# Kernel optimization log

Measured on AMD Instinct MI355X. Metric: run time of the kernel, lower is better.

## Reference

```python
import jax, jax.numpy as jnp
import numpy as np

R, T, N, OPS = 3, 3, 50000, 24
E, B, MAXDEG = 400000, 32, 8
QD, ED, H = 128, 128, 128


def lstm_scan(x, Wih, Whh, bih, bhh):
    # x: (T, B, D). PyTorch LSTM gate order: i, f, g, o.
    Hh = Whh.shape[-1]
    def step(carry, xt):
        h, c = carry
        g = xt @ Wih.T + bih + h @ Whh.T + bhh
        i, f, gg, o = jnp.split(g, 4, axis=-1)
        c = jax.nn.sigmoid(f) * c + jax.nn.sigmoid(i) * jnp.tanh(gg)
        h = jax.nn.sigmoid(o) * jnp.tanh(c)
        return (h, c), h
    z = jnp.zeros((x.shape[1], Hh), x.dtype)
    (hT, _), ys = jax.lax.scan(step, (z, z), x)
    return ys, hT


def bilstm(x, Wih, Whh, bih, bhh):
    # weights have a leading direction axis of size 2 (fwd, bwd)
    ys_f, h_f = lstm_scan(x, Wih[0], Whh[0], bih[0], bhh[0])
    ys_b, h_b = lstm_scan(x[::-1], Wih[1], Whh[1], bih[1], bhh[1])
    return jnp.concatenate([ys_f, ys_b[::-1]], -1), jnp.concatenate([h_f, h_b], -1)


def setup_inputs() -> dict:
    key = jax.random.key(0)
    ks = jax.random.split(key, 20)
    s = 0.05
    inp = {}
    inp["queries"] = jax.random.randint(ks[0], (B,), 0, OPS)
    inp["heads"] = jax.random.randint(ks[1], (B,), 0, N)
    inp["rels"] = jax.random.randint(ks[2], (E,), 0, OPS // 2)
    inp["t_heads"] = jax.random.randint(ks[3], (E,), 0, N)
    inp["t_tails"] = jax.random.randint(ks[4], (E,), 0, N)
    inp["entity_degrees"] = jax.random.randint(ks[5], (N, MAXDEG), 0, OPS + 1)
    inp["query_embedding"] = jax.random.normal(ks[6], (OPS, QD)) * s
    ent = jax.random.normal(ks[7], (OPS + 1, ED)) * s
    inp["entity_embedding"] = ent.at[OPS].set(0.0)  # padding_idx row is zero
    inp["q_Wih"] = jax.random.normal(ks[8], (R, 2, 4 * H, QD)) * s
    inp["q_Whh"] = jax.random.normal(ks[9], (R, 2, 4 * H, H)) * s
    inp["q_bih"] = jax.random.normal(ks[10], (R, 2, 4 * H)) * s
    inp["q_bhh"] = jax.random.normal(ks[11], (R, 2, 4 * H)) * s
    inp["e_Wih"] = jax.random.normal(ks[12], (2, 4 * H, ED)) * s
    inp["e_Whh"] = jax.random.normal(ks[13], (2, 4 * H, H)) * s
    inp["e_bih"] = jax.random.normal(ks[14], (2, 4 * H)) * s
    inp["e_bhh"] = jax.random.normal(ks[15], (2, 4 * H)) * s
    inp["q_lin_W"] = jax.random.normal(ks[16], (OPS + 1, 2 * H)) * s
    inp["q_lin_b"] = jax.random.normal(ks[17], (OPS + 1,)) * s
    inp["e_lin_W"] = jax.random.normal(ks[18], (OPS, 2 * H)) * s
    inp["e_lin_b"] = jax.random.normal(ks[19], (OPS,)) * s
    return inp


def reference(queries, heads, rels, t_heads, t_tails, entity_degrees,
              query_embedding, entity_embedding, q_Wih, q_Whh, q_bih, q_bhh,
              e_Wih, e_Whh, e_bih, e_bhh, q_lin_W, q_lin_b, e_lin_W, e_lin_b):
    # --- query attention over operators, one BiLSTM per rank ---
    qx = jnp.broadcast_to(query_embedding[queries][None], (T, B, QD))  # (T, B, QD)
    def q_branch(Wih, Whh, bih, bhh):
        ys, _ = bilstm(qx, Wih, Whh, bih, bhh)                 # (T, B, 2H)
        return jax.nn.softmax(ys @ q_lin_W.T + q_lin_b, axis=-1)  # (T, B, OPS+1)
    query_attn = jax.vmap(q_branch)(q_Wih, q_Whh, q_bih, q_bhh)   # (R, T, B, OPS+1)

    # --- entity attention from degree-sequence BiLSTM (final hidden states) ---
    ex = entity_embedding[entity_degrees].transpose(1, 0, 2)      # (MAXDEG, N, ED)
    _, e_h = bilstm(ex, e_Wih, e_Whh, e_bih, e_bhh)               # (N, 2H)
    entity_attn = jax.nn.softmax(e_h @ e_lin_W.T + e_lin_b, axis=-1)  # (N, OPS)

    # sparse operator values: A_rel[h, t] = entity_attn[h, rel] for fact (rel, h, t)
    w = entity_attn[t_heads, rels]  # (E,)
    half = OPS // 2

    logits = jnp.zeros((B, N), jnp.float32)
    for r in range(R):
        memory = jax.nn.one_hot(heads, N, dtype=jnp.float32)  # (B, N)
        for t in range(T):
            qa = query_attn[r, t]  # (B, OPS+1)
            # forward op: (memory @ A_rel), weighted by qa[rel]
            fwd = (qa[:, rels] * w[None, :]) * memory[:, t_heads]        # (B, E)
            # reverse op: (memory @ A_rel.T), weighted by qa[rel + half]
            rev = (qa[:, rels + half] * w[None, :]) * memory[:, t_tails]  # (B, E)
            added = (jnp.zeros((B, N), jnp.float32)
                     .at[:, t_tails].add(fwd)
                     .at[:, t_heads].add(rev))
            added = added + memory * qa[:, -1:]
            memory = added / jnp.maximum(1e-20, added.sum(axis=1, keepdims=True))
        logits = logits + memory
    return logits
```

## Files before the change

### kernel.cpp

```cpp
#include <hip/hip_runtime.h>

#define R_ 3
#define T_ 3
#define N_ 50000
#define OPS_ 24
#define E_ 400000
#define B_ 32
#define MAXDEG_ 8
#define QD_ 128
#define ED_ 128
#define H_ 128
#define G4_ (4*H_)
#define HPAD 168
#define PSLOTS 64
#define RB_ 96

#define WB_ ((2*32*5*64*8 + 511) / 512)
#define CB_ ((E_ + 511) / 512)
#define BF_ ((E_ + 511) / 512)
#define ZU_ 586
#define ZM_ 25
#define ZS_ 12
#define EB_ 16

#define QB_ (R_ * B_)
#define SCANBLK_ ((N_ + 31) / 32)
#define BF2E_ ((E_ + 511) / 512)
#define BF2N_ ((N_ + 511) / 512)

typedef unsigned short u16;
typedef unsigned char u8;
typedef __attribute__((ext_vector_type(8))) short bf16x8;
typedef __attribute__((ext_vector_type(8))) _Float16 f16x8;
typedef __attribute__((ext_vector_type(4))) float f32x4;

#define BF16_ONE ((short)0x3F80)
#define LOG2E_  1.44269504f
#define LOG2E2_ 2.88539008f

__device__ __forceinline__ short f2bf(float f){
  union { float f; unsigned u; } v; v.f = f;
  unsigned r = v.u + 0x7fffu + ((v.u >> 16) & 1u);
  return (short)(r >> 16);
}
__device__ __forceinline__ float bf2f(u16 u){
  union { unsigned u; float f; } v; v.u = ((unsigned)u) << 16; return v.f;
}
__device__ __forceinline__ float frcp(float x){ return __builtin_amdgcn_rcpf(x); }
__device__ __forceinline__ float fsig(float x){ return frcp(1.0f + __expf(-x)); }
__device__ __forceinline__ float ftanh(float x){
  return __builtin_fmaf(2.0f, fsig(2.0f * x), -1.0f);
}
__device__ __forceinline__ float fexp2(float x){
#if __has_builtin(__builtin_amdgcn_exp2f)
  return __builtin_amdgcn_exp2f(x);
#else
  return __expf(x * 0.6931471806f);
#endif
}

__device__ void qattn_body(int bid, const int* __restrict__ queries, const float* __restrict__ qemb,
    const float* __restrict__ qWih, const float* __restrict__ qWhh,
    const float* __restrict__ qbih, const float* __restrict__ qbhh,
    const float* __restrict__ qlinW, const float* __restrict__ qlinb,
    float* __restrict__ query_attn )
{
  int r = bid / B_;
  int b = bid % B_;
  int tid = threadIdx.x;
  int d   = tid >> 8;
  int t2  = tid & 255;
  __shared__ float x[QD_];
  __shared__ float gx[2][G4_];
  __shared__ float h[2][H_], c[2][H_];
  __shared__ float gtmp[2][G4_];
  __shared__ float hh[2][T_][H_];
  __shared__ float lg[OPS_ + 1];

  int q = queries[b];
  if (tid < QD_) x[tid] = qemb[q * QD_ + tid];
  __syncthreads();

  const float* Wih = qWih + (size_t)(r * 2 + d) * G4_ * QD_;
  const float* Whh = qWhh + (size_t)(r * 2 + d) * G4_ * H_;
  const float* bih = qbih + (r * 2 + d) * G4_;
  const float* bhh = qbhh + (r * 2 + d) * G4_;
  for (int j = t2; j < G4_; j += 256){
    const float4* wr = (const float4*)(Wih + (size_t)j * QD_);
    float s = bih[j] + bhh[j];
    for (int k = 0; k < QD_ / 4; ++k){
      float4 wv = wr[k];
      s += wv.x * x[4*k] + wv.y * x[4*k+1] + wv.z * x[4*k+2] + wv.w * x[4*k+3];
    }
    gx[d][j] = s;
  }
  if (t2 < H_){ h[d][t2] = 0.f; c[d][t2] = 0.f; }
  __syncthreads();
  for (int t = 0; t < T_; ++t){
    for (int j = t2; j < G4_; j += 256){
      const float4* wr = (const float4*)(Whh + (size_t)j * H_);
      float s = 0.f;
      for (int k = 0; k < H_ / 4; ++k){
        float4 wv = wr[k];
        s += wv.x * h[d][4*k] + wv.y * h[d][4*k+1] + wv.z * h[d][4*k+2] + wv.w * h[d][4*k+3];
      }
      gtmp[d][j] = gx[d][j] + s;
    }
    __syncthreads();
    if (t2 < H_){
      float gi = gtmp[d][t2], gf = gtmp[d][t2 + H_], gg = gtmp[d][t2 + 2*H_], go = gtmp[d][t2 + 3*H_];
      float cn = fsig(gf) * c[d][t2] + fsig(gi) * ftanh(gg);
      float hn = fsig(go) * ftanh(cn);
      c[d][t2] = cn; h[d][t2] = hn;
      hh[d][t][t2] = hn;
    }
    __syncthreads();
  }

  for (int t = 0; t < T_; ++t){
    if (tid < OPS_ + 1){
      const float* wr = qlinW + tid * (2 * H_);
      float s = qlinb[tid];
      for (int k = 0; k < H_; ++k) s += wr[k] * hh[0][t][k];
      for (int k = 0; k < H_; ++k) s += wr[H_ + k] * hh[1][T_ - 1 - t][k];
      lg[tid] = s;
    }
    __syncthreads();
    if (tid == 0){
      float m = -1e30f;
      for (int o = 0; o < OPS_ + 1; ++o) m = fmaxf(m, lg[o]);
      float sum = 0.f;
      for (int o = 0; o < OPS_ + 1; ++o){ float e = __expf(lg[o] - m); lg[o] = e; sum += e; }
      float inv = frcp(sum);
      for (int o = 0; o < OPS_ + 1; ++o) lg[o] *= inv;
    }
    __syncthreads();
    if (tid < OPS_ + 1) query_attn[((size_t)(r * T_ + t) * B_ + b) * (OPS_ + 1) + tid] = lg[tid];
    __syncthreads();
  }
}

__device__ void wbuild_body(int bid, const float* __restrict__ eWhh,
                            const float* __restrict__ eemb, const float* __restrict__ eWih,
                            const float* __restrict__ ebih, const float* __restrict__ ebhh,
                            u16* __restrict__ wtile, u16* __restrict__ wonehot)
{
  int idx = bid * 512 + threadIdx.x;
  if (idx >= 2 * 32 * 5 * 64 * 8) return;
  int jj = idx & 7;
  int lane = (idx >> 3) & 63;
  int kc = (idx >> 9) % 5;
  int gtile = (idx / (8 * 64 * 5)) & 31;
  int dir = idx / (8 * 64 * 5 * 32);
  int row = lane >> 4, col = lane & 15;
  int j = gtile * 16 + col;
  float sc = ((gtile >> 3) == 2) ? LOG2E2_ : LOG2E_;
  if (kc < 4){
    int k = kc * 32 + row * 8 + jj;
    float v = eWhh[((size_t)dir * G4_ + j) * H_ + k] * sc;
    wtile[((((size_t)dir * 32 + gtile) * 4 + kc) * 64 + lane) * 8 + jj] = (u16)f2bf(v);
  } else {
    int vdeg = row * 8 + jj;
    float v = 0.f;
    if (vdeg <= OPS_){
      const float4* wr = (const float4*)(eWih + (size_t)(dir * G4_ + j) * ED_);
      const float4* er = (const float4*)(eemb + (size_t)vdeg * ED_);
      float s = ebih[dir * G4_ + j] + ebhh[dir * G4_ + j];
      for (int k = 0; k < ED_ / 4; ++k){
        float4 wv = wr[k], ev = er[k];
        s += wv.x * ev.x + wv.y * ev.y + wv.z * ev.z + wv.w * ev.w;
      }
      v = s * sc;
    }
    wonehot[(((size_t)dir * 32 + gtile) * 64 + lane) * 8 + jj] = (u16)f2bf(v);
  }
}

__device__ void csr_count_body(int bid, const int* __restrict__ theads,
                               const int* __restrict__ ttails, int* __restrict__ counts)
{
  int e = bid * 512 + threadIdx.x;
  if (e < E_){
    atomicAdd(&counts[ttails[e]], 1);
    atomicAdd(&counts[theads[e]], 1);
  }
}

__device__ void bfs1_body(int bid, const int* __restrict__ heads,
                          const int* __restrict__ theads, const int* __restrict__ ttails,
                          u8* __restrict__ hs1)
{
  if (bid == 0 && threadIdx.x < B_) hs1[heads[threadIdx.x]] = 1;
  int e = bid * 512 + threadIdx.x;
  if (e < E_){
    int a = theads[e], t = ttails[e];
    #pragma unroll 8
    for (int i = 0; i < B_; ++i){
      int hd = heads[i];
      if (a == hd) hs1[t] = 1;
      if (t == hd) hs1[a] = 1;
    }
  }
}

__global__ __launch_bounds__(512) void front_kernel(
    const float* eWhh, const float* eemb, const float* eWih,
    const float* ebih, const float* ebhh, u16* wtile, u16* wonehot,
    const int* theads, const int* ttails, int* counts,
    const int* heads, u8* hs1,
    float* u2, int* maski, float* sumsP,
    const float* elinW, u16* etile)
{
  int bid = blockIdx.x;
  int tid = threadIdx.x;
  if (bid < WB_){
    wbuild_body(bid, eWhh, eemb, eWih, ebih, ebhh, wtile, wonehot);
  } else if (bid < WB_ + CB_){
    csr_count_body(bid - WB_, theads, ttails, counts);
  } else if (bid < WB_ + CB_ + BF_){
    bfs1_body(bid - WB_ - CB_, heads, theads, ttails, hs1);
  } else if (bid < WB_ + CB_ + BF_ + ZU_){
    int zb = bid - WB_ - CB_ - BF_;
    float4 z = {0.f, 0.f, 0.f, 0.f};
    size_t base = (size_t)zb * 8192 + tid * 4;
    #pragma unroll
    for (int k = 0; k < 4; ++k){
      size_t idx = base + (size_t)k * 2048;
      if (idx < (size_t)N_ * RB_) *(float4*)&u2[idx] = z;
    }
  } else if (bid < WB_ + CB_ + BF_ + ZU_ + ZM_){
    int mi = (bid - WB_ - CB_ - BF_ - ZU_) * 512 + tid;
    if (mi < (N_ + 3) / 4) maski[mi] = 0;
  } else if (bid < WB_ + CB_ + BF_ + ZU_ + ZM_ + ZS_){
    int si = (bid - WB_ - CB_ - BF_ - ZU_ - ZM_) * 512 + tid;
    if (si < PSLOTS * RB_) sumsP[si] = 0.f;
  } else {
    int idx = (bid - (WB_ + CB_ + BF_ + ZU_ + ZM_ + ZS_)) * 512 + tid;
    if (idx < 8192){
      int jj = idx & 7;
      int lane = (idx >> 3) & 63;
      int ks = (idx >> 9) & 7;
      int ot = idx >> 12;
      int op = ot * 16 + (lane & 15);
      int k  = ks * 32 + (lane >> 4) * 8 + jj;
      float v = (op < OPS_) ? elinW[(size_t)op * (2 * H_) + k] : 0.f;
      _Float16 hv = (_Float16)v;
      etile[idx] = *(const u16*)&hv;
    }
  }
}

__device__ void bfs2_body(int bid, const int* __restrict__ theads,
                          const int* __restrict__ ttails,
                          const u8* __restrict__ hs1, u8* __restrict__ mask)
{
  if (bid < BF2E_){
    int e = bid * 512 + threadIdx.x;
    if (e < E_){
      int a = theads[e], t = ttails[e];
      if (hs1[a]) mask[t] = 1;
      if (hs1[t]) mask[a] = 1;
    }
  } else {
    int n = (bid - BF2E_) * 512 + threadIdx.x;
    if (n < N_ && hs1[n]) mask[n] = 1;
  }
}

__device__ void scan_body(const int* __restrict__ counts, int* __restrict__ rowptr,
                          int* __restrict__ cursor, int* __restrict__ cursor2)
{
  __shared__ int wsum[8];
  int t = threadIdx.x;
  int lane = t & 63, wv = t >> 6;
  int carry = 0;
  for (int base = 0; base < N_; base += 2048){
    int idx = base + t * 4;
    int c0 = 0, c1 = 0, c2 = 0, c3 = 0;
    if (idx + 3 < N_){
      int4 c = *(const int4*)&counts[idx];
      c0 = c.x; c1 = c.y; c2 = c.z; c3 = c.w;
    } else {
      if (idx     < N_) c0 = counts[idx];
      if (idx + 1 < N_) c1 = counts[idx + 1];
      if (idx + 2 < N_) c2 = counts[idx + 2];
      if (idx + 3 < N_) c3 = counts[idx + 3];
    }
    int s = c0 + c1 + c2 + c3;
    int sc = s;
    #pragma unroll
    for (int off = 1; off < 64; off <<= 1){
      int v = __shfl_up(sc, off);
      if (lane >= off) sc += v;
    }
    if (lane == 63) wsum[wv] = sc;
    __syncthreads();
    if (t == 0){
      int acc = carry;
      #pragma unroll
      for (int w = 0; w < 8; ++w){ int v = wsum[w]; wsum[w] = acc; acc += v; }
      carry = acc;
    }
    __syncthreads();
    int excl = wsum[wv] + (sc - s);
    int r0 = excl, r1 = r0 + c0, r2 = r1 + c1, r3 = r2 + c2;
    if (idx + 3 < N_){
      int4 rv; rv.x = r0; rv.y = r1; rv.z = r2; rv.w = r3;
      *(int4*)&rowptr[idx]  = rv;
      *(int4*)&cursor[idx]  = rv;
      *(int4*)&cursor2[idx] = rv;
    } else {
      if (idx     < N_){ rowptr[idx]   = r0; cursor[idx]   = r0; cursor2[idx]   = r0; }
      if (idx + 1 < N_){ rowptr[idx+1] = r1; cursor[idx+1] = r1; cursor2[idx+1] = r1; }
      if (idx + 2 < N_){ rowptr[idx+2] = r2; cursor[idx+2] = r2; cursor2[idx+2] = r2; }
      if (idx + 3 < N_){ rowptr[idx+3] = r3; cursor[idx+3] = r3; cursor2[idx+3] = r3; }
    }
  }
  if (t == 0) rowptr[N_] = carry;
}

__global__ __launch_bounds__(512, 4) void elstm_kernel(
    const int* __restrict__ degs,
    const u16* __restrict__ wtile, const u16* __restrict__ wonehot,
    const u16* __restrict__ etile, const float* __restrict__ elinb,
    float* __restrict__ attn ,
    const int* __restrict__ counts, int* __restrict__ rowptr,
    int* __restrict__ cursor, int* __restrict__ cursor2,
    const int* __restrict__ theads, const int* __restrict__ ttails,
    const u8* __restrict__ hs1, u8* __restrict__ mask,
    const int* __restrict__ queries, const float* __restrict__ qemb,
    const float* __restrict__ qWih, const float* __restrict__ qWhh,
    const float* __restrict__ qbih, const float* __restrict__ qbhh,
    const float* __restrict__ qlinW, const float* __restrict__ qlinb,
    float* __restrict__ query_attn)
{
  int bid = blockIdx.x;
  if (bid < QB_){
    qattn_body(bid, queries, qemb, qWih, qWhh, qbih, qbhh, qlinW, qlinb, query_attn);
    return;
  }
  int eb = bid - QB_;
  if (eb >= SCANBLK_){
    int rid = eb - SCANBLK_;
    if (rid == 0) scan_body(counts, rowptr, cursor, cursor2);
    else          bfs2_body(rid - 1, theads, ttails, hs1, mask);
    return;
  }

  int tid = threadIdx.x;
  int lane = tid & 63;
  int w = tid >> 6;
  int wu = __builtin_amdgcn_readfirstlane(w);
  int row = lane >> 4, col = lane & 15;
  int ebase = eb * 32;

  __shared__ __align__(16) short hl[2][32 * HPAD];
  __shared__ __align__(16) short hfin[32 * 136];
  __shared__ float lgs[32][33];

  int eg0 = ebase + tid; if (eg0 >= N_) eg0 = N_ - 1;

  for (int i = tid; i < 2 * 32 * HPAD; i += 512) ((short*)hl)[i] = 0;
  __syncthreads();
  if (tid < 32) hl[0][tid * HPAD + H_ + degs[(size_t)eg0 * MAXDEG_ + 0]] = BF16_ONE;
  __syncthreads();

  int swzr = (col >> 2) & 3;

  for (int dir = 0; dir < 2; ++dir){
    const u16* Wt  = wtile   + (size_t)dir * 32 * 4 * 64 * 8;
    const u16* Woh = wonehot + (size_t)dir * 32 * 64 * 8;
    const u16* W0 = Wt + (size_t)((0 * 8 + wu) * 4 * 64) * 8;
    const u16* W1 = Wt + (size_t)((1 * 8 + wu) * 4 * 64) * 8;
    const u16* W2 = Wt + (size_t)((2 * 8 + wu) * 4 * 64) * 8;
    const u16* W3 = Wt + (size_t)((3 * 8 + wu) * 4 * 64) * 8;
    const u16* O0 = Woh + (size_t)((0 * 8 + wu) * 64) * 8;
    const u16* O1 = Woh + (size_t)((1 * 8 + wu) * 64) * 8;
    const u16* O2 = Woh + (size_t)((2 * 8 + wu) * 64) * 8;
    const u16* O3 = Woh + (size_t)((3 * 8 + wu) * 64) * 8;
    float cst[8];
    #pragma unroll
    for (int i = 0; i < 8; ++i) cst[i] = 0.f;

    for (int t = 0; t < MAXDEG_; ++t){
      const short* hb = hl[t & 1];
      short*       hw = hl[(t + 1) & 1];
      f32x4 acc[8];
      #pragma unroll
      for (int i = 0; i < 8; ++i) acc[i] = (f32x4){0.f, 0.f, 0.f, 0.f};

      #pragma unroll 2
      for (int kc = 0; kc < 4; ++kc){
        bf16x8 af0 = *(const bf16x8*)&hb[(col) * HPAD + kc * 32 + (row ^ swzr) * 8];
        bf16x8 af1 = *(const bf16x8*)&hb[(16 + col) * HPAD + kc * 32 + (row ^ swzr) * 8];
        int lo = (kc * 64 + lane) * 8;
        bf16x8 b0 = *(const bf16x8*)(W0 + lo);
        bf16x8 b1 = *(const bf16x8*)(W1 + lo);
        bf16x8 b2 = *(const bf16x8*)(W2 + lo);
        bf16x8 b3 = *(const bf16x8*)(W3 + lo);
        acc[0] = __builtin_amdgcn_mfma_f32_16x16x32_bf16(af0, b0, acc[0], 0, 0, 0);
        acc[1] = __builtin_amdgcn_mfma_f32_16x16x32_bf16(af1, b0, acc[1], 0, 0, 0);
        acc[2] = __builtin_amdgcn_mfma_f32_16x16x32_bf16(af0, b1, acc[2], 0, 0, 0);
        acc[3] = __builtin_amdgcn_mfma_f32_16x16x32_bf16(af1, b1, acc[3], 0, 0, 0);
        acc[4] = __builtin_amdgcn_mfma_f32_16x16x32_bf16(af0, b2, acc[4], 0, 0, 0);
        acc[5] = __builtin_amdgcn_mfma_f32_16x16x32_bf16(af1, b2, acc[5], 0, 0, 0);
        acc[6] = __builtin_amdgcn_mfma_f32_16x16x32_bf16(af0, b3, acc[6], 0, 0, 0);
        acc[7] = __builtin_amdgcn_mfma_f32_16x16x32_bf16(af1, b3, acc[7], 0, 0, 0);
      }
      {
        bf16x8 af0 = *(const bf16x8*)&hb[(col) * HPAD + H_ + row * 8];
        bf16x8 af1 = *(const bf16x8*)&hb[(16 + col) * HPAD + H_ + row * 8];
        int lo = lane * 8;
        bf16x8 b0 = *(const bf16x8*)(O0 + lo);
        bf16x8 b1 = *(const bf16x8*)(O1 + lo);
        bf16x8 b2 = *(const bf16x8*)(O2 + lo);
        bf16x8 b3 = *(const bf16x8*)(O3 + lo);
        acc[0] = __builtin_amdgcn_mfma_f32_16x16x32_bf16(af0, b0, acc[0], 0, 0, 0);
        acc[1] = __builtin_amdgcn_mfma_f32_16x16x32_bf16(af1, b0, acc[1], 0, 0, 0);
        acc[2] = __builtin_amdgcn_mfma_f32_16x16x32_bf16(af0, b1, acc[2], 0, 0, 0);
        acc[3] = __builtin_amdgcn_mfma_f32_16x16x32_bf16(af1, b1, acc[3], 0, 0, 0);
        acc[4] = __builtin_amdgcn_mfma_f32_16x16x32_bf16(af0, b2, acc[4], 0, 0, 0);
        acc[5] = __builtin_amdgcn_mfma_f32_16x16x32_bf16(af1, b2, acc[5], 0, 0, 0);
        acc[6] = __builtin_amdgcn_mfma_f32_16x16x32_bf16(af0, b3, acc[6], 0, 0, 0);
        acc[7] = __builtin_amdgcn_mfma_f32_16x16x32_bf16(af1, b3, acc[7], 0, 0, 0);
      }

      #pragma unroll
      for (int mt = 0; mt < 2; ++mt){
        #pragma unroll
        for (int reg = 0; reg < 4; ++reg){
          int e = mt * 16 + row * 4 + reg;
          int jsw = (((wu * 2 + (col >> 3)) ^ row) * 8) + (col & 7);
          float Gi = acc[0 + mt][reg];
          float Gf = acc[2 + mt][reg];
          float Gg = acc[4 + mt][reg];
          float Go = acc[6 + mt][reg];
          int ci = mt * 4 + reg;
          float ea = fexp2(-Gi);
          float ef = fexp2(-Gf);
          float eb2 = fexp2(-Gg);
          float eo = fexp2(-Go);
          float t1 = 1.f + ef, t2 = 1.f + ea, t3 = 1.f + eb2;
          float p = t2 * t3;
          float num = __builtin_fmaf(cst[ci], p, (1.f - eb2) * t1);
          float cn = num * frcp(t1 * p);
          float ed = fexp2(cn * (-LOG2E2_));
          float hn = (1.f - ed) * frcp((1.f + eo) * (1.f + ed));
          cst[ci] = cn;
          hw[e * HPAD + jsw] = f2bf(hn);
        }
      }
      if (tid < 32){
        const int* dr = degs + (size_t)eg0 * MAXDEG_;
        if (t >= 1)
          hw[tid * HPAD + H_ + dr[dir ? (MAXDEG_ - t) : (t - 1)]] = 0;
        if (t < MAXDEG_ - 1)
          hw[tid * HPAD + H_ + dr[dir ? (MAXDEG_ - 2 - t) : (t + 1)]] = BF16_ONE;
      }
      __syncthreads();
    }

    if (dir == 0){
      for (int i = tid; i < 32 * 16; i += 512){
        int e = i >> 4, c = i & 15;
        int sz = (e >> 2) & 3;
        *(bf16x8*)&hfin[e * 136 + c * 8] =
            *(const bf16x8*)&hl[0][e * HPAD + ((c ^ sz) * 8)];
      }
      __syncthreads();
      for (int i = tid; i < 2 * 32 * HPAD; i += 512) ((short*)hl)[i] = 0;
      __syncthreads();
      if (tid < 32) hl[0][tid * HPAD + H_ + degs[(size_t)eg0 * MAXDEG_ + (MAXDEG_ - 1)]] = BF16_ONE;
      __syncthreads();
    }
  }

  if (wu < 4){
    int mt = wu >> 1, ot = wu & 1;
    int e2 = mt * 16 + col;
    f32x4 accL = (f32x4){0.f, 0.f, 0.f, 0.f};
    #pragma unroll
    for (int ks = 0; ks < 8; ++ks){
      bf16x8 ra;
      if (ks < 4) ra = *(const bf16x8*)&hfin[e2 * 136 + ks * 32 + row * 8];
      else        ra = *(const bf16x8*)&hl[0][e2 * HPAD + (ks - 4) * 32 + (row ^ swzr) * 8];
      f16x8 af;
      #pragma unroll
      for (int jj = 0; jj < 8; ++jj) af[jj] = (_Float16)bf2f((u16)ra[jj]);
      f16x8 bfr = *(const f16x8*)(etile + (((size_t)(ot * 8 + ks)) * 64 + lane) * 8);
      accL = __builtin_amdgcn_mfma_f32_16x16x32_f16(af, bfr, accL, 0, 0, 0);
    }
    #pragma unroll
    for (int reg = 0; reg < 4; ++reg){
      int ent = mt * 16 + (lane >> 4) * 4 + reg;
      int op  = ot * 16 + (lane & 15);
      float bb = (op < OPS_) ? elinb[op] : 0.f;
      lgs[ent][op] = accL[reg] + bb;
    }
  }
  __syncthreads();
  if (tid < 32){
    int n = ebase + tid;
    if (n < N_){
      float m = -1e30f;
      #pragma unroll
      for (int o = 0; o < OPS_; ++o) m = fmaxf(m, lgs[tid][o]);
      float s = 0.f;
      #pragma unroll
      for (int o = 0; o < OPS_; ++o) s += __expf(lgs[tid][o] - m);
      float inv = frcp(s);
      #pragma unroll
      for (int o = 0; o < OPS_; ++o)
        attn[(size_t)n * OPS_ + o] = __expf(lgs[tid][o] - m) * inv;
    }
  }
}

__global__ void csr_fill_kernel(const int* __restrict__ rels, const int* __restrict__ theads,
                                const int* __restrict__ ttails, const float* __restrict__ attn,
                                const u8* __restrict__ mask, const u8* __restrict__ hs1,
                                int* __restrict__ cursor, int* __restrict__ cursor2,
                                uint2* __restrict__ ents, uint2* __restrict__ ents2)
{
  int e = blockIdx.x * 256 + threadIdx.x;
  if (e < E_){
    int hh = theads[e], tt = ttails[e];
    int mh = mask[hh], mt = mask[tt];
    if (!(mh | mt)) return;
    int rel = rels[e];
    unsigned wb = __float_as_uint(attn[(size_t)hh * OPS_ + rel]);
    if (mh){
      uint2 v1; v1.x = (unsigned)hh | ((unsigned)rel << 16); v1.y = wb;
      ents[atomicAdd(&cursor[tt], 1)] = v1;
    }
    if (mt){
      uint2 v2; v2.x = (unsigned)tt | ((unsigned)(rel + OPS_/2) << 16); v2.y = wb;
      ents[atomicAdd(&cursor[hh], 1)] = v2;
    }
    if (hs1[hh]){
      uint2 w1; w1.x = (unsigned)tt | ((unsigned)rel << 16); w1.y = wb;
      ents2[atomicAdd(&cursor2[hh], 1)] = w1;
    }
    if (hs1[tt]){
      uint2 w2; w2.x = (unsigned)hh | ((unsigned)(rel + OPS_/2) << 16); w2.y = wb;
      ents2[atomicAdd(&cursor2[tt], 1)] = w2;
    }
  }
}

__global__ void t01_kernel(const int* __restrict__ heads, const float* __restrict__ query_attn,
                           const int* __restrict__ rowptr, const int* __restrict__ cend2,
                           const uint2* __restrict__ ents2, float* __restrict__ u2)
{
  __shared__ float qa0[OPS_ + 1], qa1[OPS_ + 1];
  int blk = blockIdx.x;
  int r = blk >> 5, b = blk & 31;
  int rb = r * 32 + b;
  int tid = threadIdx.x;
  if (tid < OPS_ + 1){
    qa0[tid] = query_attn[((size_t)(r * T_ + 0) * B_ + b) * (OPS_ + 1) + tid];
    qa1[tid] = query_attn[((size_t)(r * T_ + 1) * B_ + b) * (OPS_ + 1) + tid];
  }
  __syncthreads();
  int hd = heads[b];
  int beg = rowptr[hd], end = cend2[hd];
  float q024 = qa0[OPS_], q124 = qa1[OPS_];
  if (tid == 0) atomicAdd(&u2[(size_t)hd * RB_ + rb], q124 * q024);
  for (int i = beg + tid; i < end; i += 64){
    uint2 e1 = ents2[i];
    int s  = (int)(e1.x & 0xFFFFu);
    int r1 = (int)(e1.x >> 16);
    float w1 = __uint_as_float(e1.y);
    atomicAdd(&u2[(size_t)s * RB_ + rb], w1 * (q124 * qa0[r1] + qa1[r1] * q024));
    float v1 = qa0[r1] * w1;
    int b2 = rowptr[s], e2e = cend2[s];
    for (int jj = b2; jj < e2e; ++jj){
      uint2 e2 = ents2[jj];
      int d2 = (int)(e2.x & 0xFFFFu);
      int r2 = (int)(e2.x >> 16);
      atomicAdd(&u2[(size_t)d2 * RB_ + rb], qa1[r2] * __uint_as_float(e2.y) * v1);
    }
  }
}

__global__ __launch_bounds__(256) void gather3_kernel(
    const float* __restrict__ ucur, float* __restrict__ unxt,
    const float* __restrict__ query_attn, int t,
    const int* __restrict__ rowptr, const int* __restrict__ cend,
    const uint2* __restrict__ ents, const u8* __restrict__ mask,
    float* __restrict__ partial )
{
  __shared__ float qas[3 * B_ * (OPS_ + 1)];
  __shared__ float red[RB_];
  int tid = threadIdx.x;
  for (int i = tid; i < 3 * B_ * (OPS_ + 1); i += 256){
    int r = i / (B_ * (OPS_ + 1));
    int rem = i - r * (B_ * (OPS_ + 1));
    qas[i] = query_attn[(size_t)(r * T_ + t) * B_ * (OPS_ + 1) + rem];
  }
  if (tid < RB_) red[tid] = 0.f;
  __syncthreads();
  int b   = tid & 31;
  int hw2 = tid >> 5;
  const float* q0 = &qas[0 * 800 + b * (OPS_ + 1)];
  const float* q1 = &qas[1 * 800 + b * (OPS_ + 1)];
  const float* q2 = &qas[2 * 800 + b * (OPS_ + 1)];
  float s0a = 0.f, s1a = 0.f, s2a = 0.f;
  for (int n = blockIdx.x * 8 + hw2; n < N_; n += gridDim.x * 8){
    int beg = rowptr[n], end = cend[n];
    int mk = mask[n];
    if (end == beg && !mk) continue;
    size_t nb = (size_t)n * RB_;
    float a0 = 0.f, a1 = 0.f, a2 = 0.f;
    if (mk){
      a0 = ucur[nb + b]      * q0[OPS_];
      a1 = ucur[nb + 32 + b] * q1[OPS_];
      a2 = ucur[nb + 64 + b] * q2[OPS_];
    }
    #pragma unroll 2
    for (int i = beg; i < end; ++i){
      uint2 e0 = ents[i];
      size_t s0 = (size_t)(e0.x & 0xFFFFu) * RB_;
      int r0 = (int)(e0.x >> 16);
      float w0 = __uint_as_float(e0.y);
      a0 += q0[r0] * w0 * ucur[s0 + b];
      a1 += q1[r0] * w0 * ucur[s0 + 32 + b];
      a2 += q2[r0] * w0 * ucur[s0 + 64 + b];
    }
    unxt[nb + b]      = a0;
    unxt[nb + 32 + b] = a1;
    unxt[nb + 64 + b] = a2;
    s0a += a0; s1a += a1; s2a += a2;
  }
  atomicAdd(&red[b], s0a);
  atomicAdd(&red[32 + b], s1a);
  atomicAdd(&red[64 + b], s2a);
  __syncthreads();
  if (tid < RB_)
    atomicAdd(&partial[(blockIdx.x & (PSLOTS - 1)) * RB_ + tid], red[tid]);
}

__global__ void fintrans_kernel(const float* __restrict__ u, const float* __restrict__ partial,
                                const int* __restrict__ rowptr, const int* __restrict__ cend,
                                const u8* __restrict__ mask,
                                float* __restrict__ out)
{
  __shared__ float sinv[RB_];
  __shared__ float t[B_][72];
  int tid = threadIdx.x;
  if (tid < RB_){
    float s = 0.f;
    #pragma unroll 8
    for (int k = 0; k < PSLOTS; ++k) s += partial[k * RB_ + tid];
    sinv[tid] = frcp(fmaxf(1e-20f, s));
  }
  __syncthreads();
  int n0 = blockIdx.x * 64;
  for (int i = tid; i < 64 * B_; i += 256){
    int nl = i >> 5, b = i & 31;
    int n = n0 + nl;
    float v = 0.f;
    if (n < N_ && (mask[n] || cend[n] > rowptr[n])){
      size_t nb = (size_t)n * RB_;
      v = u[nb + b] * sinv[b] + u[nb + 32 + b] * sinv[32 + b] + u[nb + 64 + b] * sinv[64 + b];
    }
    t[b][nl] = v;
  }
  __syncthreads();
  for (int i = tid; i < 64 * B_; i += 256){
    int b = i >> 6, nl = i & 63;
    int n = n0 + nl;
    if (n < N_) out[(size_t)b * N_ + n] = t[b][nl];
  }
}

extern "C" void kernel_launch(void* const* d_in, const int* in_sizes, int n_in,
                              void* d_out, int out_size, void* d_ws, size_t ws_size,
                              hipStream_t stream)
{
  const int*   queries = (const int*)d_in[0];
  const int*   heads   = (const int*)d_in[1];
  const int*   rels    = (const int*)d_in[2];
  const int*   t_heads = (const int*)d_in[3];
  const int*   t_tails = (const int*)d_in[4];
  const int*   edeg    = (const int*)d_in[5];
  const float* qemb    = (const float*)d_in[6];
  const float* eemb    = (const float*)d_in[7];
  const float* qWih    = (const float*)d_in[8];
  const float* qWhh    = (const float*)d_in[9];
  const float* qbih    = (const float*)d_in[10];
  const float* qbhh    = (const float*)d_in[11];
  const float* eWih    = (const float*)d_in[12];
  const float* eWhh    = (const float*)d_in[13];
  const float* ebih    = (const float*)d_in[14];
  const float* ebhh    = (const float*)d_in[15];
  const float* qlinW   = (const float*)d_in[16];
  const float* qlinb   = (const float*)d_in[17];
  const float* elinW   = (const float*)d_in[18];
  const float* elinb   = (const float*)d_in[19];
  float* out = (float*)d_out;

  char* ws = (char*)d_ws;
  size_t off = 0;
  auto alloc = [&](size_t bytes){ void* p = ws + off; off += (bytes + 255) & ~(size_t)255; return p; };
  char*  bigB  = (char*)alloc((size_t)N_ * RB_ * 4);
  float* attn  = (float*)bigB;
  float* u3    = (float*)bigB;
  uint2* ents       = (uint2*)alloc((size_t)2 * E_ * 8);
  float* u2         = (float*)alloc((size_t)N_ * RB_ * 4);
  uint2* ents2      = (uint2*)alloc((size_t)2 * E_ * 8);
  float* query_attn = (float*)alloc((size_t)R_ * T_ * B_ * (OPS_ + 1) * 4);
  u16*   wtile      = (u16*)  alloc((size_t)2 * 32 * 4 * 64 * 8 * 2);
  u16*   wonehot    = (u16*)  alloc((size_t)2 * 32 * 64 * 8 * 2);
  u16*   etile      = (u16*)  alloc((size_t)2 * 8 * 64 * 8 * 2);
  int*   counts     = (int*)  alloc((size_t)(N_ + 1) * 4);
  int*   rowptr     = (int*)  alloc((size_t)(N_ + 1) * 4);
  int*   cursor     = (int*)  alloc((size_t)(N_ + 1) * 4);
  int*   cursor2    = (int*)  alloc((size_t)(N_ + 1) * 4);
  u8*    hs1        = (u8*)   alloc((size_t)N_);
  u8*    mask       = (u8*)   alloc((size_t)N_);
  float* sumsP      = (float*)alloc((size_t)PSLOTS * RB_ * 4);

  hipMemsetAsync(counts, 0, (size_t)(N_ + 1) * 4, stream);
  hipMemsetAsync(hs1, 0, (size_t)N_, stream);

  front_kernel<<<WB_ + CB_ + BF_ + ZU_ + ZM_ + ZS_ + EB_, 512, 0, stream>>>(
      eWhh, eemb, eWih, ebih, ebhh, wtile, wonehot,
      t_heads, t_tails, counts, heads, hs1, u2, (int*)mask, sumsP, elinW, etile);
  elstm_kernel<<<QB_ + SCANBLK_ + 1 + BF2E_ + BF2N_, 512, 0, stream>>>(
      edeg, wtile, wonehot, etile, elinb, attn,
      counts, rowptr, cursor, cursor2,
      t_heads, t_tails, hs1, mask,
      queries, qemb, qWih, qWhh, qbih, qbhh, qlinW, qlinb, query_attn);
  csr_fill_kernel<<<(E_ + 255) / 256, 256, 0, stream>>>(rels, t_heads, t_tails, attn,
                                                        mask, hs1, cursor, cursor2,
                                                        ents, ents2);
  t01_kernel<<<RB_, 64, 0, stream>>>(heads, query_attn, rowptr, cursor2, ents2, u2);
  gather3_kernel<<<1024, 256, 0, stream>>>(u2, u3, query_attn, 2, rowptr, cursor,
                                           ents, mask, sumsP);
  fintrans_kernel<<<(N_ + 63) / 64, 256, 0, stream>>>(u3, sumsP, rowptr, cursor,
                                                      mask, out);
}
```

Baseline: 423.2 us.

## Compact 2-hop frontier state into dense index space for cache locality

The byte mask becomes an int mask, set with atomicCAS, and each newly reached frontier node gets a compact index from an atomic counter. The two-hop state u2 is written and read through this compact index, so gather3 touches a dense, smaller working set instead of rows scattered over all N nodes. The cost is extra atomics in the frontier pass, one more indirection load per edge in gather3 and t01, and a mask four times wider. The u2 zeroing still clears the full N-sized buffer.

```diff
diff --git a/kernel.cpp b/kernel.cpp
--- a/kernel.cpp
+++ b/kernel.cpp
@@ -19,7 +19,7 @@
 #define CB_ ((E_ + 511) / 512)
 #define BF_ ((E_ + 511) / 512)
 #define ZU_ 586
-#define ZM_ 25
+#define ZM_ ((N_ + 511) / 512)
 #define ZS_ 12
 #define EB_ 16
 
@@ -230,7 +230,7 @@
     }
   } else if (bid < WB_ + CB_ + BF_ + ZU_ + ZM_){
     int mi = (bid - WB_ - CB_ - BF_ - ZU_) * 512 + tid;
-    if (mi < (N_ + 3) / 4) maski[mi] = 0;
+    if (mi < N_) maski[mi] = 0;
   } else if (bid < WB_ + CB_ + BF_ + ZU_ + ZM_ + ZS_){
     int si = (bid - WB_ - CB_ - BF_ - ZU_ - ZM_) * 512 + tid;
     if (si < PSLOTS * RB_) sumsP[si] = 0.f;
@@ -252,18 +252,19 @@
 
 __device__ void bfs2_body(int bid, const int* __restrict__ theads,
                           const int* __restrict__ ttails,
-                          const u8* __restrict__ hs1, u8* __restrict__ mask)
+                          const u8* __restrict__ hs1, int* __restrict__ mask,
+                          int* __restrict__ cidx, int* __restrict__ cnt)
 {
   if (bid < BF2E_){
     int e = bid * 512 + threadIdx.x;
     if (e < E_){
       int a = theads[e], t = ttails[e];
-      if (hs1[a]) mask[t] = 1;
-      if (hs1[t]) mask[a] = 1;
+      if (hs1[a] && atomicCAS(&mask[t], 0, 1) == 0) cidx[t] = atomicAdd(cnt, 1);
+      if (hs1[t] && atomicCAS(&mask[a], 0, 1) == 0) cidx[a] = atomicAdd(cnt, 1);
     }
   } else {
     int n = (bid - BF2E_) * 512 + threadIdx.x;
-    if (n < N_ && hs1[n]) mask[n] = 1;
+    if (n < N_ && hs1[n] && atomicCAS(&mask[n], 0, 1) == 0) cidx[n] = atomicAdd(cnt, 1);
   }
 }
 
@@ -324,10 +325,10 @@
     const u16* __restrict__ wtile, const u16* __restrict__ wonehot,
     const u16* __restrict__ etile, const float* __restrict__ elinb,
     float* __restrict__ attn ,
-    const int* __restrict__ counts, int* __restrict__ rowptr,
+    int* __restrict__ counts, int* __restrict__ rowptr,
     int* __restrict__ cursor, int* __restrict__ cursor2,
     const int* __restrict__ theads, const int* __restrict__ ttails,
-    const u8* __restrict__ hs1, u8* __restrict__ mask,
+    const u8* __restrict__ hs1, int* __restrict__ mask, int* __restrict__ cidx,
     const int* __restrict__ queries, const float* __restrict__ qemb,
     const float* __restrict__ qWih, const float* __restrict__ qWhh,
     const float* __restrict__ qbih, const float* __restrict__ qbhh,
@@ -343,7 +344,7 @@
   if (eb >= SCANBLK_){
     int rid = eb - SCANBLK_;
     if (rid == 0) scan_body(counts, rowptr, cursor, cursor2);
-    else          bfs2_body(rid - 1, theads, ttails, hs1, mask);
+    else          bfs2_body(rid - 1, theads, ttails, hs1, mask, cidx, &counts[N_]);
     return;
   }
 
@@ -518,7 +519,7 @@
 
 __global__ void csr_fill_kernel(const int* __restrict__ rels, const int* __restrict__ theads,
                                 const int* __restrict__ ttails, const float* __restrict__ attn,
-                                const u8* __restrict__ mask, const u8* __restrict__ hs1,
+                                const int* __restrict__ mask, const u8* __restrict__ hs1,
                                 int* __restrict__ cursor, int* __restrict__ cursor2,
                                 uint2* __restrict__ ents, uint2* __restrict__ ents2)
 {
@@ -550,7 +551,8 @@
 
 __global__ void t01_kernel(const int* __restrict__ heads, const float* __restrict__ query_attn,
                            const int* __restrict__ rowptr, const int* __restrict__ cend2,
-                           const uint2* __restrict__ ents2, float* __restrict__ u2)
+                           const uint2* __restrict__ ents2, const int* __restrict__ cidx,
+                           float* __restrict__ u2c)
 {
   __shared__ float qa0[OPS_ + 1], qa1[OPS_ + 1];
   int blk = blockIdx.x;
@@ -565,29 +567,30 @@
   int hd = heads[b];
   int beg = rowptr[hd], end = cend2[hd];
   float q024 = qa0[OPS_], q124 = qa1[OPS_];
-  if (tid == 0) atomicAdd(&u2[(size_t)hd * RB_ + rb], q124 * q024);
+  if (tid == 0) atomicAdd(&u2c[(size_t)cidx[hd] * RB_ + rb], q124 * q024);
   for (int i = beg + tid; i < end; i += 64){
     uint2 e1 = ents2[i];
     int s  = (int)(e1.x & 0xFFFFu);
     int r1 = (int)(e1.x >> 16);
     float w1 = __uint_as_float(e1.y);
-    atomicAdd(&u2[(size_t)s * RB_ + rb], w1 * (q124 * qa0[r1] + qa1[r1] * q024));
+    atomicAdd(&u2c[(size_t)cidx[s] * RB_ + rb], w1 * (q124 * qa0[r1] + qa1[r1] * q024));
     float v1 = qa0[r1] * w1;
     int b2 = rowptr[s], e2e = cend2[s];
     for (int jj = b2; jj < e2e; ++jj){
       uint2 e2 = ents2[jj];
       int d2 = (int)(e2.x & 0xFFFFu);
       int r2 = (int)(e2.x >> 16);
-      atomicAdd(&u2[(size_t)d2 * RB_ + rb], qa1[r2] * __uint_as_float(e2.y) * v1);
+      atomicAdd(&u2c[(size_t)cidx[d2] * RB_ + rb], qa1[r2] * __uint_as_float(e2.y) * v1);
     }
   }
 }
 
 __global__ __launch_bounds__(256) void gather3_kernel(
-    const float* __restrict__ ucur, float* __restrict__ unxt,
+    const float* __restrict__ ucur_c, float* __restrict__ unxt,
     const float* __restrict__ query_attn, int t,
     const int* __restrict__ rowptr, const int* __restrict__ cend,
-    const uint2* __restrict__ ents, const u8* __restrict__ mask,
+    const uint2* __restrict__ ents, const int* __restrict__ mask,
+    const int* __restrict__ cidx,
     float* __restrict__ partial )
 {
   __shared__ float qas[3 * B_ * (OPS_ + 1)];
@@ -613,19 +616,20 @@
     size_t nb = (size_t)n * RB_;
     float a0 = 0.f, a1 = 0.f, a2 = 0.f;
     if (mk){
-      a0 = ucur[nb + b]      * q0[OPS_];
-      a1 = ucur[nb + 32 + b] * q1[OPS_];
-      a2 = ucur[nb + 64 + b] * q2[OPS_];
+      size_t cb = (size_t)cidx[n] * RB_;
+      a0 = ucur_c[cb + b]      * q0[OPS_];
+      a1 = ucur_c[cb + 32 + b] * q1[OPS_];
+      a2 = ucur_c[cb + 64 + b] * q2[OPS_];
     }
     #pragma unroll 2
     for (int i = beg; i < end; ++i){
       uint2 e0 = ents[i];
-      size_t s0 = (size_t)(e0.x & 0xFFFFu) * RB_;
+      size_t s0 = (size_t)cidx[e0.x & 0xFFFFu] * RB_;
       int r0 = (int)(e0.x >> 16);
       float w0 = __uint_as_float(e0.y);
-      a0 += q0[r0] * w0 * ucur[s0 + b];
-      a1 += q1[r0] * w0 * ucur[s0 + 32 + b];
-      a2 += q2[r0] * w0 * ucur[s0 + 64 + b];
+      a0 += q0[r0] * w0 * ucur_c[s0 + b];
+      a1 += q1[r0] * w0 * ucur_c[s0 + 32 + b];
+      a2 += q2[r0] * w0 * ucur_c[s0 + 64 + b];
     }
     unxt[nb + b]      = a0;
     unxt[nb + 32 + b] = a1;
@@ -642,7 +646,7 @@
 
 __global__ void fintrans_kernel(const float* __restrict__ u, const float* __restrict__ partial,
                                 const int* __restrict__ rowptr, const int* __restrict__ cend,
-                                const u8* __restrict__ mask,
+                                const int* __restrict__ mask,
                                 float* __restrict__ out)
 {
   __shared__ float sinv[RB_];
@@ -718,7 +722,8 @@
   int*   cursor     = (int*)  alloc((size_t)(N_ + 1) * 4);
   int*   cursor2    = (int*)  alloc((size_t)(N_ + 1) * 4);
   u8*    hs1        = (u8*)   alloc((size_t)N_);
-  u8*    mask       = (u8*)   alloc((size_t)N_);
+  int*   mask       = (int*)  alloc((size_t)N_ * 4);
+  int*   cidx       = (int*)  alloc((size_t)N_ * 4);
   float* sumsP      = (float*)alloc((size_t)PSLOTS * RB_ * 4);
 
   hipMemsetAsync(counts, 0, (size_t)(N_ + 1) * 4, stream);
@@ -726,18 +731,19 @@
 
   front_kernel<<<WB_ + CB_ + BF_ + ZU_ + ZM_ + ZS_ + EB_, 512, 0, stream>>>(
       eWhh, eemb, eWih, ebih, ebhh, wtile, wonehot,
-      t_heads, t_tails, counts, heads, hs1, u2, (int*)mask, sumsP, elinW, etile);
+      t_heads, t_tails, counts, heads, hs1, u2, mask, sumsP, elinW, etile);
   elstm_kernel<<<QB_ + SCANBLK_ + 1 + BF2E_ + BF2N_, 512, 0, stream>>>(
       edeg, wtile, wonehot, etile, elinb, attn,
       counts, rowptr, cursor, cursor2,
-      t_heads, t_tails, hs1, mask,
+      t_heads, t_tails, hs1, mask, cidx,
       queries, qemb, qWih, qWhh, qbih, qbhh, qlinW, qlinb, query_attn);
   csr_fill_kernel<<<(E_ + 255) / 256, 256, 0, stream>>>(rels, t_heads, t_tails, attn,
                                                         mask, hs1, cursor, cursor2,
                                                         ents, ents2);
-  t01_kernel<<<RB_, 64, 0, stream>>>(heads, query_attn, rowptr, cursor2, ents2, u2);
+  t01_kernel<<<RB_, 64, 0, stream>>>(heads, query_attn, rowptr, cursor2, ents2,
+                                     cidx, u2);
   gather3_kernel<<<1024, 256, 0, stream>>>(u2, u3, query_attn, 2, rowptr, cursor,
-                                           ents, mask, sumsP);
+                                           ents, mask, cidx, sumsP);
   fintrans_kernel<<<(N_ + 63) / 64, 256, 0, stream>>>(u3, sumsP, rowptr, cursor,
                                                       mask, out);
 }
```

Measured after the change: 483.6 us. +14.3%, slower.
